# Optimization experiments

Hardware: AMD Instinct MI355X
Metric: run time of the kernel (lower is better)

Reference implementation:

```python
import jax, jax.numpy as jnp
import numpy as np

H = 8          # num_heads
D = 64         # out_dims = input_dims / num_heads
DM = H * D     # input_dims = 512
B, S = 2, 2048


def _linear(x, W, b):
    # torch nn.Linear: x @ W.T + b, W: [out, in]
    return jnp.einsum('...d,ed->...e', x, W) + b


def setup_inputs() -> dict:
    key = jax.random.key(0)
    ks = jax.random.split(key, 12)
    inp = {
        'query': jax.random.normal(ks[0], (B, S, DM), dtype=jnp.float32),
        'key': jax.random.normal(ks[1], (B, S, DM), dtype=jnp.float32),
        'value': jax.random.normal(ks[2], (B, S, DM), dtype=jnp.float32),
        'Wq': jax.random.normal(ks[3], (D, D), dtype=jnp.float32) * 0.02,
        'bq': jnp.zeros((D,), dtype=jnp.float32),
        'Wk': jax.random.normal(ks[4], (D, D), dtype=jnp.float32) * 0.02,
        'bk': jnp.zeros((D,), dtype=jnp.float32),
        'Wv': jax.random.normal(ks[5], (D, D), dtype=jnp.float32) * 0.02,
        'bv': jnp.zeros((D,), dtype=jnp.float32),
        'Wo': jax.random.normal(ks[6], (DM, DM), dtype=jnp.float32) * 0.02,
        'bo': jnp.zeros((DM,), dtype=jnp.float32),
        'mask': jax.random.randint(ks[7], (B, 1, 1, S), 0, 2, dtype=jnp.int32),
    }
    return inp


def reference(query, key, value, Wq, bq, Wk, bk, Wv, bv, Wo, bo, mask):
    b, qlen = query.shape[0], query.shape[1]
    klen = key.shape[1]
    # split heads: [B, S, H, D]
    q = _linear(query.reshape(b, qlen, H, D), Wq, bq)
    k = _linear(key.reshape(b, klen, H, D), Wk, bk)
    v = _linear(value.reshape(b, klen, H, D), Wv, bv)
    # scores: [B, H, Q, K]
    attn = jnp.einsum('bqhd,bkhd->bhqk', q, k)
    attn = jnp.where(mask == 0, jnp.float32(-1e20), attn)
    # NOTE: original scale is num_heads ** 1 / 2 == H / 2 (Python precedence quirk)
    score = jax.nn.softmax(attn * (2.0 / H), axis=-1)
    # out einsum gives [B, Q, D, H]; flattening gives (d, h) feature order
    out = jnp.einsum('bhqv,bvhd->bqdh', score, v)
    out = out.reshape(b, qlen, D * H)
    return _linear(out, Wo, bo)
```

## Files before the change

kernel.cpp:

```cpp
#include <hip/hip_runtime.h>
#include <math.h>

typedef float f32x4 __attribute__((ext_vector_type(4)));
typedef short s16x8 __attribute__((ext_vector_type(8)));
typedef unsigned short ushort_t;

namespace {
constexpr int kH  = 8;
constexpr int kD  = 64;
constexpr int kDM = 512;
constexpr int kB  = 2;
constexpr int kS  = 2048;
constexpr size_t kNE = (size_t)kB * kH * kS * kD;
}

__device__ __forceinline__ void split_bf16(float x, ushort_t& hi, ushort_t& lo) {
  union { float f; unsigned u; } a; a.f = x;
  hi = (ushort_t)(a.u >> 16);
  union { unsigned u; float f; } hh; hh.u = a.u & 0xffff0000u;
  union { float f; unsigned u; } r; r.f = x - hh.f;
  lo = (ushort_t)(r.u >> 16);
}

__global__ __launch_bounds__(256)
void wo_split_kernel(const float* __restrict__ Wo,
                     ushort_t* __restrict__ wh, ushort_t* __restrict__ wl) {
  const int i = (blockIdx.x * 256 + threadIdx.x) * 4;
  float4 v = *(const float4*)&Wo[i];
  ushort_t h[4], l[4];
  split_bf16(v.x, h[0], l[0]);
  split_bf16(v.y, h[1], l[1]);
  split_bf16(v.z, h[2], l[2]);
  split_bf16(v.w, h[3], l[3]);
  int2 hp, lp;
  hp.x = (int)((unsigned)h[0] | ((unsigned)h[1] << 16));
  hp.y = (int)((unsigned)h[2] | ((unsigned)h[3] << 16));
  lp.x = (int)((unsigned)l[0] | ((unsigned)l[1] << 16));
  lp.y = (int)((unsigned)l[2] | ((unsigned)l[3] << 16));
  *(int2*)&wh[i] = hp;
  *(int2*)&wl[i] = lp;
}

__global__ __launch_bounds__(256, 4)
void qkv_proj_kernel(const float* __restrict__ xq, const float* __restrict__ xk,
                     const float* __restrict__ xv,
                     const float* __restrict__ Wq, const float* __restrict__ bq,
                     const float* __restrict__ Wk, const float* __restrict__ bk,
                     const float* __restrict__ Wv, const float* __restrict__ bv,
                     ushort_t* __restrict__ q_hi, ushort_t* __restrict__ q_lo,
                     ushort_t* __restrict__ k_hi,
                     ushort_t* __restrict__ vt_hi, ushort_t* __restrict__ vt_lo) {
  __shared__ __align__(16) float Xs[32][68];
  __shared__ __align__(16) float Ws[64][68];
  const int h = blockIdx.y;
  const int which = blockIdx.z;
  const float* x; const float* W; const float* bias;
  if (which == 0)      { x = xq; W = Wq; bias = bq; }
  else if (which == 1) { x = xk; W = Wk; bias = bk; }
  else                 { x = xv; W = Wv; bias = bv; }
  const int t0 = blockIdx.x * 32;
  const int tid = threadIdx.x;

  for (int idx = tid; idx < 32 * 16; idx += 256) {
    int r = idx >> 4, c = idx & 15;
    *(float4*)&Xs[r][c * 4] =
        *(const float4*)&x[(size_t)(t0 + r) * kDM + h * kD + c * 4];
  }
  for (int idx = tid; idx < 64 * 16; idx += 256) {
    int r = idx >> 4, c = idx & 15;
    *(float4*)&Ws[r][c * 4] = *(const float4*)&W[(size_t)r * kD + c * 4];
  }
  __syncthreads();

  const int tok = tid >> 3;
  const int ec  = tid & 7;
  float acc[8] = {0.f, 0.f, 0.f, 0.f, 0.f, 0.f, 0.f, 0.f};
  #pragma unroll
  for (int d4 = 0; d4 < 16; ++d4) {
    float4 xv4 = *(const float4*)&Xs[tok][d4 * 4];
    #pragma unroll
    for (int j = 0; j < 8; ++j) {
      float4 wv = *(const float4*)&Ws[ec + 8 * j][d4 * 4];
      acc[j] = fmaf(xv4.x, wv.x, acc[j]);
      acc[j] = fmaf(xv4.y, wv.y, acc[j]);
      acc[j] = fmaf(xv4.z, wv.z, acc[j]);
      acc[j] = fmaf(xv4.w, wv.w, acc[j]);
    }
  }
  __syncthreads();

  ushort_t* Hs = (ushort_t*)Xs;
  ushort_t* Ls = (ushort_t*)Ws;

  const int b = (t0 >> 11);
  const int s0 = t0 & (kS - 1);
  const size_t hb = ((size_t)b * kH + h) * (size_t)(kS * kD);

  if (which < 2) {
    #pragma unroll
    for (int j = 0; j < 8; ++j) {
      const int e = ec + 8 * j;
      ushort_t hi, lo;
      split_bf16(acc[j] + bias[e], hi, lo);
      Hs[tok * 72 + e] = hi;
      if (which == 0) Ls[tok * 72 + e] = lo;
    }
  } else {
    #pragma unroll
    for (int j = 0; j < 8; ++j) {
      const int e = ec + 8 * j;
      ushort_t hi, lo;
      split_bf16(acc[j] + bias[e], hi, lo);
      Hs[e * 40 + tok] = hi;
      Ls[e * 40 + tok] = lo;
    }
  }
  __syncthreads();

  if (which < 2) {
    const int r = tid >> 3, c = tid & 7;
    ushort_t* dh = (which == 0) ? q_hi : k_hi;
    *(int4*)&dh[hb + (size_t)(s0 + r) * kD + c * 8] = *(int4*)&Hs[r * 72 + c * 8];
    if (which == 0)
      *(int4*)&q_lo[hb + (size_t)(s0 + r) * kD + c * 8] = *(int4*)&Ls[r * 72 + c * 8];
  } else {
    const int r = tid >> 2, c = tid & 3;
    *(int4*)&vt_hi[hb + (size_t)r * kS + s0 + c * 8] = *(int4*)&Hs[r * 40 + c * 8];
    *(int4*)&vt_lo[hb + (size_t)r * kS + s0 + c * 8] = *(int4*)&Ls[r * 40 + c * 8];
  }
}

__global__ __launch_bounds__(256, 2)
void attn_kernel(const ushort_t* __restrict__ q_hi, const ushort_t* __restrict__ q_lo,
                 const ushort_t* __restrict__ k_hi,
                 const ushort_t* __restrict__ vt_hi, const ushort_t* __restrict__ vt_lo,
                 const int* __restrict__ mask,
                 ushort_t* __restrict__ ctx_h, ushort_t* __restrict__ ctx_l) {
  __shared__ __align__(16) ushort_t Kh[64][72];
  __shared__ __align__(16) ushort_t Vh[64][72];
  __shared__ __align__(16) ushort_t Vl[64][72];
  __shared__ __align__(16) unsigned P32[4][16][68];
  __shared__ float Mz[64];

  const int tid  = threadIdx.x;
  const int w    = tid >> 6;
  const int lane = tid & 63;
  const int ln   = lane & 15;
  const int quad = lane >> 4;
  const int h = blockIdx.y, b = blockIdx.z;
  const int q0 = blockIdx.x * 64;
  const size_t hb = ((size_t)b * kH + h) * (size_t)(kS * kD);

  const int qrow = q0 + w * 16 + ln;
  s16x8 aqh[2], aql[2];
  #pragma unroll
  for (int db = 0; db < 2; ++db) {
    aqh[db] = *(const s16x8*)&q_hi[hb + (size_t)qrow * kD + db * 32 + quad * 8];
    aql[db] = *(const s16x8*)&q_lo[hb + (size_t)qrow * kD + db * 32 + quad * 8];
  }

  f32x4 O[4];
  #pragma unroll
  for (int db = 0; db < 4; ++db) O[db] = (f32x4){0.f, 0.f, 0.f, 0.f};
  float rs[4] = {0.f, 0.f, 0.f, 0.f};

  for (int kt = 0; kt < kS / 64; ++kt) {
    __syncthreads();
    {
      const ushort_t* gkh = k_hi + hb + (size_t)kt * 64 * kD;
      const ushort_t* gvh = vt_hi + hb + (size_t)kt * 64;
      const ushort_t* gvl = vt_lo + hb + (size_t)kt * 64;
      #pragma unroll
      for (int cc = 0; cc < 2; ++cc) {
        const int c = tid + cc * 256;
        const int r = c >> 3, off = (c & 7) * 8;
        *(int4*)&Kh[r][off] = *(const int4*)&gkh[r * kD + off];
        *(int4*)&Vh[r][off] = *(const int4*)&gvh[(size_t)r * kS + off];
        *(int4*)&Vl[r][off] = *(const int4*)&gvl[(size_t)r * kS + off];
      }
      if (tid < 64) Mz[tid] = (mask[(size_t)b * kS + kt * 64 + tid] != 0) ? 1.0f : 0.0f;
    }
    __syncthreads();

    f32x4 C[4];
    #pragma unroll
    for (int kb = 0; kb < 4; ++kb) C[kb] = (f32x4){0.f, 0.f, 0.f, 0.f};
    #pragma unroll
    for (int db = 0; db < 2; ++db) {
      s16x8 bh[4];
      #pragma unroll
      for (int kb = 0; kb < 4; ++kb)
        bh[kb] = *(const s16x8*)&Kh[kb * 16 + ln][db * 32 + quad * 8];
      #pragma unroll
      for (int kb = 0; kb < 4; ++kb)
        C[kb] = __builtin_amdgcn_mfma_f32_16x16x32_bf16(aqh[db], bh[kb], C[kb], 0, 0, 0);
      #pragma unroll
      for (int kb = 0; kb < 4; ++kb)
        C[kb] = __builtin_amdgcn_mfma_f32_16x16x32_bf16(aql[db], bh[kb], C[kb], 0, 0, 0);
    }

    #pragma unroll
    for (int kb = 0; kb < 4; ++kb) {
      const float mz = Mz[kb * 16 + ln];
      #pragma unroll
      for (int r = 0; r < 4; ++r) {
        const float p = mz * __expf(0.25f * C[kb][r]);
        rs[r] += p;
        ushort_t hi, lo;
        split_bf16(p, hi, lo);
        P32[w][quad * 4 + r][kb * 16 + ln] = ((unsigned)hi << 16) | (unsigned)lo;
      }
    }

    #pragma unroll
    for (int kh = 0; kh < 2; ++kh) {
      const int4 u0 = *(const int4*)&P32[w][ln][kh * 32 + quad * 8];
      const int4 u1 = *(const int4*)&P32[w][ln][kh * 32 + quad * 8 + 4];
      const unsigned uu[8] = {(unsigned)u0.x, (unsigned)u0.y, (unsigned)u0.z, (unsigned)u0.w,
                              (unsigned)u1.x, (unsigned)u1.y, (unsigned)u1.z, (unsigned)u1.w};
      s16x8 ph, pl;
      #pragma unroll
      for (int j = 0; j < 8; ++j) {
        ph[j] = (short)(uu[j] >> 16);
        pl[j] = (short)(uu[j] & 0xffffu);
      }
      s16x8 vh[4], vl[4];
      #pragma unroll
      for (int db = 0; db < 4; ++db) {
        vh[db] = *(const s16x8*)&Vh[db * 16 + ln][kh * 32 + quad * 8];
        vl[db] = *(const s16x8*)&Vl[db * 16 + ln][kh * 32 + quad * 8];
      }
      #pragma unroll
      for (int db = 0; db < 4; ++db)
        O[db] = __builtin_amdgcn_mfma_f32_16x16x32_bf16(ph, vh[db], O[db], 0, 0, 0);
      #pragma unroll
      for (int db = 0; db < 4; ++db)
        O[db] = __builtin_amdgcn_mfma_f32_16x16x32_bf16(ph, vl[db], O[db], 0, 0, 0);
      #pragma unroll
      for (int db = 0; db < 4; ++db)
        O[db] = __builtin_amdgcn_mfma_f32_16x16x32_bf16(pl, vh[db], O[db], 0, 0, 0);
    }
  }

  #pragma unroll
  for (int m = 1; m < 16; m <<= 1) {
    #pragma unroll
    for (int r = 0; r < 4; ++r) rs[r] += __shfl_xor(rs[r], m);
  }
  float inv[4];
  #pragma unroll
  for (int r = 0; r < 4; ++r) inv[r] = 1.0f / rs[r];

  #pragma unroll
  for (int db = 0; db < 4; ++db) {
    const int d = db * 16 + ln;
    #pragma unroll
    for (int r = 0; r < 4; ++r) {
      const int qg = q0 + w * 16 + quad * 4 + r;
      const size_t o = ((size_t)b * kS + qg) * kDM + d * kH + h;
      ushort_t hi, lo;
      split_bf16(O[db][r] * inv[r], hi, lo);
      ctx_h[o] = hi;
      ctx_l[o] = lo;
    }
  }
}

__global__ __launch_bounds__(256, 2)
void out_proj_kernel(const ushort_t* __restrict__ ch, const ushort_t* __restrict__ cl,
                     const ushort_t* __restrict__ wh, const ushort_t* __restrict__ wl,
                     const float* __restrict__ bo, float* __restrict__ out) {
  __shared__ __align__(16) ushort_t Ah[64][72];
  __shared__ __align__(16) ushort_t Al[64][72];
  __shared__ __align__(16) ushort_t Bh[64][72];
  __shared__ __align__(16) ushort_t Bl[64][72];
  const int t0 = blockIdx.x * 64;
  const int e0 = blockIdx.y * 64;
  const int tid  = threadIdx.x;
  const int w    = tid >> 6;
  const int lane = tid & 63;
  const int ln   = lane & 15;
  const int quad = lane >> 4;

  f32x4 C[4];
  #pragma unroll
  for (int eb = 0; eb < 4; ++eb) C[eb] = (f32x4){0.f, 0.f, 0.f, 0.f};

  for (int k0 = 0; k0 < kDM; k0 += 64) {
    __syncthreads();
    #pragma unroll
    for (int cc = 0; cc < 2; ++cc) {
      const int c = tid + cc * 256;
      const int r = c >> 3, off = (c & 7) * 8;
      *(int4*)&Ah[r][off] = *(const int4*)&ch[(size_t)(t0 + r) * kDM + k0 + off];
      *(int4*)&Al[r][off] = *(const int4*)&cl[(size_t)(t0 + r) * kDM + k0 + off];
      *(int4*)&Bh[r][off] = *(const int4*)&wh[(size_t)(e0 + r) * kDM + k0 + off];
      *(int4*)&Bl[r][off] = *(const int4*)&wl[(size_t)(e0 + r) * kDM + k0 + off];
    }
    __syncthreads();
    #pragma unroll
    for (int kc = 0; kc < 2; ++kc) {
      const s16x8 ah = *(const s16x8*)&Ah[w * 16 + ln][kc * 32 + quad * 8];
      const s16x8 al = *(const s16x8*)&Al[w * 16 + ln][kc * 32 + quad * 8];
      s16x8 bh[4], bl[4];
      #pragma unroll
      for (int eb = 0; eb < 4; ++eb) {
        bh[eb] = *(const s16x8*)&Bh[eb * 16 + ln][kc * 32 + quad * 8];
        bl[eb] = *(const s16x8*)&Bl[eb * 16 + ln][kc * 32 + quad * 8];
      }
      #pragma unroll
      for (int eb = 0; eb < 4; ++eb)
        C[eb] = __builtin_amdgcn_mfma_f32_16x16x32_bf16(ah, bh[eb], C[eb], 0, 0, 0);
      #pragma unroll
      for (int eb = 0; eb < 4; ++eb)
        C[eb] = __builtin_amdgcn_mfma_f32_16x16x32_bf16(ah, bl[eb], C[eb], 0, 0, 0);
      #pragma unroll
      for (int eb = 0; eb < 4; ++eb)
        C[eb] = __builtin_amdgcn_mfma_f32_16x16x32_bf16(al, bh[eb], C[eb], 0, 0, 0);
    }
  }

  #pragma unroll
  for (int eb = 0; eb < 4; ++eb) {
    const int e = e0 + eb * 16 + ln;
    const float be = bo[e];
    #pragma unroll
    for (int r = 0; r < 4; ++r) {
      const int t = t0 + w * 16 + quad * 4 + r;
      out[(size_t)t * kDM + e] = C[eb][r] + be;
    }
  }
}

extern "C" void kernel_launch(void* const* d_in, const int* in_sizes, int n_in,
                              void* d_out, int out_size, void* d_ws, size_t ws_size,
                              hipStream_t stream) {
  const float* query = (const float*)d_in[0];
  const float* key   = (const float*)d_in[1];
  const float* value = (const float*)d_in[2];
  const float* Wq = (const float*)d_in[3];
  const float* bq = (const float*)d_in[4];
  const float* Wk = (const float*)d_in[5];
  const float* bk = (const float*)d_in[6];
  const float* Wv = (const float*)d_in[7];
  const float* bv = (const float*)d_in[8];
  const float* Wo = (const float*)d_in[9];
  const float* bo = (const float*)d_in[10];
  const int* mask = (const int*)d_in[11];
  float* out = (float*)d_out;

  ushort_t* q_hi  = (ushort_t*)d_ws;
  ushort_t* q_lo  = q_hi + kNE;
  ushort_t* k_hi  = q_lo + kNE;
  ushort_t* vt_hi = k_hi + kNE;
  ushort_t* vt_lo = vt_hi + kNE;
  ushort_t* ctx_h = vt_lo + kNE;
  ushort_t* ctx_l = ctx_h + kNE;
  ushort_t* wo_h  = ctx_l + kNE;
  ushort_t* wo_l  = wo_h + (size_t)kDM * kDM;

  wo_split_kernel<<<dim3(kDM * kDM / 1024), 256, 0, stream>>>(Wo, wo_h, wo_l);
  qkv_proj_kernel<<<dim3(kB * kS / 32, kH, 3), 256, 0, stream>>>(
      query, key, value, Wq, bq, Wk, bk, Wv, bv,
      q_hi, q_lo, k_hi, vt_hi, vt_lo);
  attn_kernel<<<dim3(kS / 64, kH, kB), 256, 0, stream>>>(
      q_hi, q_lo, k_hi, vt_hi, vt_lo, mask, ctx_h, ctx_l);
  out_proj_kernel<<<dim3(kB * kS / 64, kDM / 64), 256, 0, stream>>>(
      ctx_h, ctx_l, wo_h, wo_l, bo, out);
}
```

Baseline: 189.7 us.

## Fuse Q projection into attention, use split-bf16 MFMA for K/V projections

Moves the Q projection into the attention kernel, so Q is computed on chip from fp32 input and the q_hi/q_lo global round trip goes away. The K/V projections switch from scalar fp32 FMA to three-term split-bf16 MFMA, with weights pre-split by a combined weight-split kernel. Context output is staged through shared memory and written as coalesced int4 rows. To keep this consistent, Wo columns are permuted at split time to match the new (h,d) context ordering. Risks are extra shared-memory staging and syncs in attention, plus accuracy changes from the three-term bf16 product.

```diff
diff --git a/kernel.cpp b/kernel.cpp
--- a/kernel.cpp
+++ b/kernel.cpp
@@ -23,115 +23,167 @@
 }
 
 __global__ __launch_bounds__(256)
-void wo_split_kernel(const float* __restrict__ Wo,
-                     ushort_t* __restrict__ wh, ushort_t* __restrict__ wl) {
-  const int i = (blockIdx.x * 256 + threadIdx.x) * 4;
-  float4 v = *(const float4*)&Wo[i];
-  ushort_t h[4], l[4];
-  split_bf16(v.x, h[0], l[0]);
-  split_bf16(v.y, h[1], l[1]);
-  split_bf16(v.z, h[2], l[2]);
-  split_bf16(v.w, h[3], l[3]);
-  int2 hp, lp;
-  hp.x = (int)((unsigned)h[0] | ((unsigned)h[1] << 16));
-  hp.y = (int)((unsigned)h[2] | ((unsigned)h[3] << 16));
-  lp.x = (int)((unsigned)l[0] | ((unsigned)l[1] << 16));
-  lp.y = (int)((unsigned)l[2] | ((unsigned)l[3] << 16));
-  *(int2*)&wh[i] = hp;
-  *(int2*)&wl[i] = lp;
-}
-
-__global__ __launch_bounds__(256, 4)
-void qkv_proj_kernel(const float* __restrict__ xq, const float* __restrict__ xk,
-                     const float* __restrict__ xv,
-                     const float* __restrict__ Wq, const float* __restrict__ bq,
-                     const float* __restrict__ Wk, const float* __restrict__ bk,
-                     const float* __restrict__ Wv, const float* __restrict__ bv,
-                     ushort_t* __restrict__ q_hi, ushort_t* __restrict__ q_lo,
-                     ushort_t* __restrict__ k_hi,
-                     ushort_t* __restrict__ vt_hi, ushort_t* __restrict__ vt_lo) {
-  __shared__ __align__(16) float Xs[32][68];
-  __shared__ __align__(16) float Ws[64][68];
+void w_split_kernel(const float* __restrict__ Wo, const float* __restrict__ Wq,
+                    const float* __restrict__ Wk, const float* __restrict__ Wv,
+                    ushort_t* __restrict__ wo_h, ushort_t* __restrict__ wo_l,
+                    ushort_t* __restrict__ wq_h, ushort_t* __restrict__ wq_l,
+                    ushort_t* __restrict__ wk_h, ushort_t* __restrict__ wk_l,
+                    ushort_t* __restrict__ wv_h, ushort_t* __restrict__ wv_l) {
+  const int bid = blockIdx.x;
+  if (bid < 256) {
+    const int i = (bid * 256 + threadIdx.x) * 4;
+    const float4 v = *(const float4*)&Wo[i];
+    const int e = i >> 9;
+    const float vv[4] = {v.x, v.y, v.z, v.w};
+    #pragma unroll
+    for (int j = 0; j < 4; ++j) {
+      const int f = (i & 511) + j;
+      const int g = (f & 7) * 64 + (f >> 3);
+      ushort_t hi, lo;
+      split_bf16(vv[j], hi, lo);
+      wo_h[(size_t)e * kDM + g] = hi;
+      wo_l[(size_t)e * kDM + g] = lo;
+    }
+  } else {
+    const int which = bid - 256;
+    const float* W = (which == 0) ? Wq : (which == 1) ? Wk : Wv;
+    ushort_t* oh = (which == 0) ? wq_h : (which == 1) ? wk_h : wv_h;
+    ushort_t* ol = (which == 0) ? wq_l : (which == 1) ? wk_l : wv_l;
+    #pragma unroll
+    for (int cc = 0; cc < 4; ++cc) {
+      const int i = (cc * 256 + threadIdx.x) * 4;
+      const float4 v = *(const float4*)&W[i];
+      ushort_t h[4], l[4];
+      split_bf16(v.x, h[0], l[0]);
+      split_bf16(v.y, h[1], l[1]);
+      split_bf16(v.z, h[2], l[2]);
+      split_bf16(v.w, h[3], l[3]);
+      int2 hp, lp;
+      hp.x = (int)((unsigned)h[0] | ((unsigned)h[1] << 16));
+      hp.y = (int)((unsigned)h[2] | ((unsigned)h[3] << 16));
+      lp.x = (int)((unsigned)l[0] | ((unsigned)l[1] << 16));
+      lp.y = (int)((unsigned)l[2] | ((unsigned)l[3] << 16));
+      *(int2*)&oh[i] = hp;
+      *(int2*)&ol[i] = lp;
+    }
+  }
+}
+
+__global__ __launch_bounds__(256, 2)
+void kv_proj_kernel(const float* __restrict__ xk, const float* __restrict__ xv,
+                    const ushort_t* __restrict__ wk_h, const ushort_t* __restrict__ wk_l,
+                    const float* __restrict__ bk,
+                    const ushort_t* __restrict__ wv_h, const ushort_t* __restrict__ wv_l,
+                    const float* __restrict__ bv,
+                    ushort_t* __restrict__ k_hi,
+                    ushort_t* __restrict__ vt_hi, ushort_t* __restrict__ vt_lo) {
+  __shared__ __align__(16) ushort_t Xh[64][72];
+  __shared__ __align__(16) ushort_t Xl[64][72];
+  const int which = blockIdx.z;
+  const float* x = which ? xv : xk;
+  const ushort_t* wh = which ? wv_h : wk_h;
+  const ushort_t* wl = which ? wv_l : wk_l;
+  const float* bias = which ? bv : bk;
   const int h = blockIdx.y;
-  const int which = blockIdx.z;
-  const float* x; const float* W; const float* bias;
-  if (which == 0)      { x = xq; W = Wq; bias = bq; }
-  else if (which == 1) { x = xk; W = Wk; bias = bk; }
-  else                 { x = xv; W = Wv; bias = bv; }
-  const int t0 = blockIdx.x * 32;
-  const int tid = threadIdx.x;
-
-  for (int idx = tid; idx < 32 * 16; idx += 256) {
-    int r = idx >> 4, c = idx & 15;
-    *(float4*)&Xs[r][c * 4] =
-        *(const float4*)&x[(size_t)(t0 + r) * kDM + h * kD + c * 4];
-  }
-  for (int idx = tid; idx < 64 * 16; idx += 256) {
-    int r = idx >> 4, c = idx & 15;
-    *(float4*)&Ws[r][c * 4] = *(const float4*)&W[(size_t)r * kD + c * 4];
+  const int t0g = blockIdx.x * 64;
+  const int b = t0g >> 11, s0 = t0g & (kS - 1);
+  const int tid  = threadIdx.x;
+  const int w    = tid >> 6;
+  const int lane = tid & 63;
+  const int ln   = lane & 15;
+  const int quad = lane >> 4;
+  const size_t hb = ((size_t)b * kH + h) * (size_t)(kS * kD);
+
+  #pragma unroll
+  for (int cc = 0; cc < 4; ++cc) {
+    const int id = tid + cc * 256;
+    const int r = id >> 4, c = id & 15;
+    const float4 v = *(const float4*)&x[((size_t)t0g + r) * kDM + h * kD + c * 4];
+    ushort_t hh[4], ll[4];
+    split_bf16(v.x, hh[0], ll[0]);
+    split_bf16(v.y, hh[1], ll[1]);
+    split_bf16(v.z, hh[2], ll[2]);
+    split_bf16(v.w, hh[3], ll[3]);
+    int2 hp, lp;
+    hp.x = (int)((unsigned)hh[0] | ((unsigned)hh[1] << 16));
+    hp.y = (int)((unsigned)hh[2] | ((unsigned)hh[3] << 16));
+    lp.x = (int)((unsigned)ll[0] | ((unsigned)ll[1] << 16));
+    lp.y = (int)((unsigned)ll[2] | ((unsigned)ll[3] << 16));
+    *(int2*)&Xh[r][c * 4] = hp;
+    *(int2*)&Xl[r][c * 4] = lp;
   }
   __syncthreads();
 
-  const int tok = tid >> 3;
-  const int ec  = tid & 7;
-  float acc[8] = {0.f, 0.f, 0.f, 0.f, 0.f, 0.f, 0.f, 0.f};
-  #pragma unroll
-  for (int d4 = 0; d4 < 16; ++d4) {
-    float4 xv4 = *(const float4*)&Xs[tok][d4 * 4];
-    #pragma unroll
-    for (int j = 0; j < 8; ++j) {
-      float4 wv = *(const float4*)&Ws[ec + 8 * j][d4 * 4];
-      acc[j] = fmaf(xv4.x, wv.x, acc[j]);
-      acc[j] = fmaf(xv4.y, wv.y, acc[j]);
-      acc[j] = fmaf(xv4.z, wv.z, acc[j]);
-      acc[j] = fmaf(xv4.w, wv.w, acc[j]);
-    }
+  f32x4 C[4];
+  #pragma unroll
+  for (int eb = 0; eb < 4; ++eb) C[eb] = (f32x4){0.f, 0.f, 0.f, 0.f};
+  #pragma unroll
+  for (int kc = 0; kc < 2; ++kc) {
+    const s16x8 ah = *(const s16x8*)&Xh[w * 16 + ln][kc * 32 + quad * 8];
+    const s16x8 al = *(const s16x8*)&Xl[w * 16 + ln][kc * 32 + quad * 8];
+    s16x8 bh[4], bl[4];
+    #pragma unroll
+    for (int eb = 0; eb < 4; ++eb) {
+      bh[eb] = *(const s16x8*)&wh[(size_t)(eb * 16 + ln) * kD + kc * 32 + quad * 8];
+      bl[eb] = *(const s16x8*)&wl[(size_t)(eb * 16 + ln) * kD + kc * 32 + quad * 8];
+    }
+    #pragma unroll
+    for (int eb = 0; eb < 4; ++eb)
+      C[eb] = __builtin_amdgcn_mfma_f32_16x16x32_bf16(ah, bh[eb], C[eb], 0, 0, 0);
+    #pragma unroll
+    for (int eb = 0; eb < 4; ++eb)
+      C[eb] = __builtin_amdgcn_mfma_f32_16x16x32_bf16(ah, bl[eb], C[eb], 0, 0, 0);
+    #pragma unroll
+    for (int eb = 0; eb < 4; ++eb)
+      C[eb] = __builtin_amdgcn_mfma_f32_16x16x32_bf16(al, bh[eb], C[eb], 0, 0, 0);
   }
   __syncthreads();
 
-  ushort_t* Hs = (ushort_t*)Xs;
-  ushort_t* Ls = (ushort_t*)Ws;
-
-  const int b = (t0 >> 11);
-  const int s0 = t0 & (kS - 1);
-  const size_t hb = ((size_t)b * kH + h) * (size_t)(kS * kD);
-
-  if (which < 2) {
-    #pragma unroll
-    for (int j = 0; j < 8; ++j) {
-      const int e = ec + 8 * j;
-      ushort_t hi, lo;
-      split_bf16(acc[j] + bias[e], hi, lo);
-      Hs[tok * 72 + e] = hi;
-      if (which == 0) Ls[tok * 72 + e] = lo;
+  if (which == 0) {
+    #pragma unroll
+    for (int eb = 0; eb < 4; ++eb) {
+      const float be = bias[eb * 16 + ln];
+      #pragma unroll
+      for (int r = 0; r < 4; ++r) {
+        ushort_t hi, lo;
+        split_bf16(C[eb][r] + be, hi, lo);
+        Xh[w * 16 + quad * 4 + r][eb * 16 + ln] = hi;
+      }
+    }
+    __syncthreads();
+    #pragma unroll
+    for (int cc = 0; cc < 2; ++cc) {
+      const int id = tid + cc * 256;
+      const int r = id >> 3, c = id & 7;
+      *(int4*)&k_hi[hb + (size_t)(s0 + r) * kD + c * 8] = *(int4*)&Xh[r][c * 8];
     }
   } else {
     #pragma unroll
-    for (int j = 0; j < 8; ++j) {
-      const int e = ec + 8 * j;
-      ushort_t hi, lo;
-      split_bf16(acc[j] + bias[e], hi, lo);
-      Hs[e * 40 + tok] = hi;
-      Ls[e * 40 + tok] = lo;
-    }
-  }
-  __syncthreads();
-
-  if (which < 2) {
-    const int r = tid >> 3, c = tid & 7;
-    ushort_t* dh = (which == 0) ? q_hi : k_hi;
-    *(int4*)&dh[hb + (size_t)(s0 + r) * kD + c * 8] = *(int4*)&Hs[r * 72 + c * 8];
-    if (which == 0)
-      *(int4*)&q_lo[hb + (size_t)(s0 + r) * kD + c * 8] = *(int4*)&Ls[r * 72 + c * 8];
-  } else {
-    const int r = tid >> 2, c = tid & 3;
-    *(int4*)&vt_hi[hb + (size_t)r * kS + s0 + c * 8] = *(int4*)&Hs[r * 40 + c * 8];
-    *(int4*)&vt_lo[hb + (size_t)r * kS + s0 + c * 8] = *(int4*)&Ls[r * 40 + c * 8];
+    for (int eb = 0; eb < 4; ++eb) {
+      const float be = bias[eb * 16 + ln];
+      #pragma unroll
+      for (int r = 0; r < 4; ++r) {
+        ushort_t hi, lo;
+        split_bf16(C[eb][r] + be, hi, lo);
+        Xh[eb * 16 + ln][w * 16 + quad * 4 + r] = hi;
+        Xl[eb * 16 + ln][w * 16 + quad * 4 + r] = lo;
+      }
+    }
+    __syncthreads();
+    #pragma unroll
+    for (int cc = 0; cc < 2; ++cc) {
+      const int id = tid + cc * 256;
+      const int r = id >> 3, c = id & 7;
+      *(int4*)&vt_hi[hb + (size_t)r * kS + s0 + c * 8] = *(int4*)&Xh[r][c * 8];
+      *(int4*)&vt_lo[hb + (size_t)r * kS + s0 + c * 8] = *(int4*)&Xl[r][c * 8];
+    }
   }
 }
 
 __global__ __launch_bounds__(256, 2)
-void attn_kernel(const ushort_t* __restrict__ q_hi, const ushort_t* __restrict__ q_lo,
+void attn_kernel(const float* __restrict__ xq,
+                 const ushort_t* __restrict__ wq_h, const ushort_t* __restrict__ wq_l,
+                 const float* __restrict__ bq,
                  const ushort_t* __restrict__ k_hi,
                  const ushort_t* __restrict__ vt_hi, const ushort_t* __restrict__ vt_lo,
                  const int* __restrict__ mask,
@@ -151,12 +203,69 @@
   const int q0 = blockIdx.x * 64;
   const size_t hb = ((size_t)b * kH + h) * (size_t)(kS * kD);
 
-  const int qrow = q0 + w * 16 + ln;
+  #pragma unroll
+  for (int cc = 0; cc < 4; ++cc) {
+    const int id = tid + cc * 256;
+    const int r = id >> 4, c = id & 15;
+    const float4 v =
+        *(const float4*)&xq[((size_t)b * kS + q0 + r) * kDM + h * kD + c * 4];
+    ushort_t hh[4], ll[4];
+    split_bf16(v.x, hh[0], ll[0]);
+    split_bf16(v.y, hh[1], ll[1]);
+    split_bf16(v.z, hh[2], ll[2]);
+    split_bf16(v.w, hh[3], ll[3]);
+    int2 hp, lp;
+    hp.x = (int)((unsigned)hh[0] | ((unsigned)hh[1] << 16));
+    hp.y = (int)((unsigned)hh[2] | ((unsigned)hh[3] << 16));
+    lp.x = (int)((unsigned)ll[0] | ((unsigned)ll[1] << 16));
+    lp.y = (int)((unsigned)ll[2] | ((unsigned)ll[3] << 16));
+    *(int2*)&Kh[r][c * 4] = hp;
+    *(int2*)&Vh[r][c * 4] = lp;
+  }
+  __syncthreads();
+  {
+    f32x4 C[4];
+    #pragma unroll
+    for (int eb = 0; eb < 4; ++eb) C[eb] = (f32x4){0.f, 0.f, 0.f, 0.f};
+    #pragma unroll
+    for (int kc = 0; kc < 2; ++kc) {
+      const s16x8 ah = *(const s16x8*)&Kh[w * 16 + ln][kc * 32 + quad * 8];
+      const s16x8 al = *(const s16x8*)&Vh[w * 16 + ln][kc * 32 + quad * 8];
+      s16x8 bh[4], bl[4];
+      #pragma unroll
+      for (int eb = 0; eb < 4; ++eb) {
+        bh[eb] = *(const s16x8*)&wq_h[(size_t)(eb * 16 + ln) * kD + kc * 32 + quad * 8];
+        bl[eb] = *(const s16x8*)&wq_l[(size_t)(eb * 16 + ln) * kD + kc * 32 + quad * 8];
+      }
+      #pragma unroll
+      for (int eb = 0; eb < 4; ++eb)
+        C[eb] = __builtin_amdgcn_mfma_f32_16x16x32_bf16(ah, bh[eb], C[eb], 0, 0, 0);
+      #pragma unroll
+      for (int eb = 0; eb < 4; ++eb)
+        C[eb] = __builtin_amdgcn_mfma_f32_16x16x32_bf16(ah, bl[eb], C[eb], 0, 0, 0);
+      #pragma unroll
+      for (int eb = 0; eb < 4; ++eb)
+        C[eb] = __builtin_amdgcn_mfma_f32_16x16x32_bf16(al, bh[eb], C[eb], 0, 0, 0);
+    }
+    __syncthreads();
+    #pragma unroll
+    for (int eb = 0; eb < 4; ++eb) {
+      const float be = bq[eb * 16 + ln];
+      #pragma unroll
+      for (int r = 0; r < 4; ++r) {
+        ushort_t hi, lo;
+        split_bf16(C[eb][r] + be, hi, lo);
+        Kh[w * 16 + quad * 4 + r][eb * 16 + ln] = hi;
+        Vh[w * 16 + quad * 4 + r][eb * 16 + ln] = lo;
+      }
+    }
+    __syncthreads();
+  }
   s16x8 aqh[2], aql[2];
   #pragma unroll
   for (int db = 0; db < 2; ++db) {
-    aqh[db] = *(const s16x8*)&q_hi[hb + (size_t)qrow * kD + db * 32 + quad * 8];
-    aql[db] = *(const s16x8*)&q_lo[hb + (size_t)qrow * kD + db * 32 + quad * 8];
+    aqh[db] = *(const s16x8*)&Kh[w * 16 + ln][db * 32 + quad * 8];
+    aql[db] = *(const s16x8*)&Vh[w * 16 + ln][db * 32 + quad * 8];
   }
 
   f32x4 O[4];
@@ -251,18 +360,25 @@
   #pragma unroll
   for (int r = 0; r < 4; ++r) inv[r] = 1.0f / rs[r];
 
+  __syncthreads();
   #pragma unroll
   for (int db = 0; db < 4; ++db) {
-    const int d = db * 16 + ln;
     #pragma unroll
     for (int r = 0; r < 4; ++r) {
-      const int qg = q0 + w * 16 + quad * 4 + r;
-      const size_t o = ((size_t)b * kS + qg) * kDM + d * kH + h;
       ushort_t hi, lo;
       split_bf16(O[db][r] * inv[r], hi, lo);
-      ctx_h[o] = hi;
-      ctx_l[o] = lo;
-    }
+      Kh[w * 16 + quad * 4 + r][db * 16 + ln] = hi;
+      Vh[w * 16 + quad * 4 + r][db * 16 + ln] = lo;
+    }
+  }
+  __syncthreads();
+  #pragma unroll
+  for (int cc = 0; cc < 2; ++cc) {
+    const int id = tid + cc * 256;
+    const int r = id >> 3, c = id & 7;
+    const size_t o = ((size_t)b * kS + q0 + r) * kDM + h * kD + c * 8;
+    *(int4*)&ctx_h[o] = *(int4*)&Kh[r][c * 8];
+    *(int4*)&ctx_l[o] = *(int4*)&Vh[r][c * 8];
   }
 }
 
@@ -349,22 +465,26 @@
   const int* mask = (const int*)d_in[11];
   float* out = (float*)d_out;
 
-  ushort_t* q_hi  = (ushort_t*)d_ws;
-  ushort_t* q_lo  = q_hi + kNE;
-  ushort_t* k_hi  = q_lo + kNE;
+  ushort_t* k_hi  = (ushort_t*)d_ws;
   ushort_t* vt_hi = k_hi + kNE;
   ushort_t* vt_lo = vt_hi + kNE;
   ushort_t* ctx_h = vt_lo + kNE;
   ushort_t* ctx_l = ctx_h + kNE;
   ushort_t* wo_h  = ctx_l + kNE;
   ushort_t* wo_l  = wo_h + (size_t)kDM * kDM;
-
-  wo_split_kernel<<<dim3(kDM * kDM / 1024), 256, 0, stream>>>(Wo, wo_h, wo_l);
-  qkv_proj_kernel<<<dim3(kB * kS / 32, kH, 3), 256, 0, stream>>>(
-      query, key, value, Wq, bq, Wk, bk, Wv, bv,
-      q_hi, q_lo, k_hi, vt_hi, vt_lo);
+  ushort_t* wq_h  = wo_l + (size_t)kDM * kDM;
+  ushort_t* wq_l  = wq_h + kD * kD;
+  ushort_t* wk_h  = wq_l + kD * kD;
+  ushort_t* wk_l  = wk_h + kD * kD;
+  ushort_t* wv_h  = wk_l + kD * kD;
+  ushort_t* wv_l  = wv_h + kD * kD;
+
+  w_split_kernel<<<dim3(259), 256, 0, stream>>>(
+      Wo, Wq, Wk, Wv, wo_h, wo_l, wq_h, wq_l, wk_h, wk_l, wv_h, wv_l);
+  kv_proj_kernel<<<dim3(kB * kS / 64, kH, 2), 256, 0, stream>>>(
+      key, value, wk_h, wk_l, bk, wv_h, wv_l, bv, k_hi, vt_hi, vt_lo);
   attn_kernel<<<dim3(kS / 64, kH, kB), 256, 0, stream>>>(
-      q_hi, q_lo, k_hi, vt_hi, vt_lo, mask, ctx_h, ctx_l);
+      query, wq_h, wq_l, bq, k_hi, vt_hi, vt_lo, mask, ctx_h, ctx_l);
   out_proj_kernel<<<dim3(kB * kS / 64, kDM / 64), 256, 0, stream>>>(
       ctx_h, ctx_l, wo_h, wo_l, bo, out);
 }
```

Result: faster. 183.6 us (-3.2%).
